# Kernel tuning notes

Hardware: AMD Instinct MI355X
Metric: run time of the kernel (lower is better)

## Reference

```python
import jax, jax.numpy as jnp
import numpy as np

D_IN = 2048
D_OUT = 2048
NUM_HEADS = 16
HEAD_DIM = D_OUT // NUM_HEADS  # 128
LATENT_DIM = 256
B, S = 2, 2048


def setup_inputs() -> dict:
    key = jax.random.key(0)
    ks = jax.random.split(key, 7)
    scale = 0.02
    return {
        "x": jax.random.normal(ks[0], (B, S, D_IN), dtype=jnp.float32),
        "W_query": jax.random.normal(ks[1], (D_IN, D_OUT), dtype=jnp.float32) * scale,
        "W_DKV": jax.random.normal(ks[2], (D_IN, LATENT_DIM), dtype=jnp.float32) * scale,
        "W_UKV": jax.random.normal(ks[3], (LATENT_DIM, 2 * D_OUT), dtype=jnp.float32) * scale,
        "W_out": jax.random.normal(ks[4], (D_OUT, D_IN), dtype=jnp.float32) * scale,
        "b_out": jax.random.normal(ks[5], (D_IN,), dtype=jnp.float32) * scale,
        "offset": 0,
    }


def reference(x, W_query, W_DKV, W_UKV, W_out, b_out, offset):
    Bq, Sq, _ = x.shape
    # projections
    q = x @ W_query                      # [B, S, d_out]
    latent = x @ W_DKV                   # [B, S, latent_dim]
    kv = latent @ W_UKV                  # [B, S, 2*d_out]
    k, v = jnp.split(kv, 2, axis=-1)     # each [B, S, d_out]

    def to_heads(t):
        return t.reshape(Bq, Sq, NUM_HEADS, HEAD_DIM).transpose(0, 2, 1, 3)  # [B, H, S, hd]

    qh, kh, vh = to_heads(q), to_heads(k), to_heads(v)

    scores = jnp.einsum("bhqd,bhkd->bhqk", qh, kh)  # [B, H, S, S]
    causal = jnp.tril(jnp.ones((Sq, Sq), dtype=bool))  # True = keep (kv_cache=None -> Sq==Skv)
    # faithful to original: masked_fill(-inf) BEFORE the rsqrt(head_dim) scaling
    scores = jnp.where(causal, scores, -jnp.inf)
    inv_sqrt_d = jax.lax.rsqrt(jnp.asarray(HEAD_DIM, dtype=scores.dtype))
    attn = jax.nn.softmax(scores * inv_sqrt_d, axis=-1)  # dropout p=0 -> identity

    ctx = jnp.einsum("bhqk,bhkd->bhqd", attn, vh)        # [B, H, S, hd]
    ctx = ctx.transpose(0, 2, 1, 3).reshape(Bq, Sq, D_OUT)
    return ctx @ W_out + b_out           # [B, S, d_in]
```

## Files before the change

### kernel.cpp

```cpp
#include <hip/hip_runtime.h>
#include <hip/hip_bf16.h>

typedef short bf16x8 __attribute__((ext_vector_type(8)));
typedef float f32x4 __attribute__((ext_vector_type(4)));
typedef float f32x16 __attribute__((ext_vector_type(16)));
typedef unsigned int u32x4 __attribute__((ext_vector_type(4)));
typedef unsigned short u16;
typedef unsigned short u16x4 __attribute__((ext_vector_type(4)));
typedef unsigned short u16x8 __attribute__((ext_vector_type(8)));

constexpr int D_IN = 2048, D_OUT = 2048, NH = 16, HD = 128, LAT = 256;
constexpr int Bb = 2, Ss = 2048, Mtot = Bb * Ss;

constexpr float QSCALE = 0.08838834764831845f * 1.4426950408889634f;
constexpr float NEG_BIG = -3.0e38f;

__device__ __forceinline__ u16 f2bf(float f) {
  unsigned u = __float_as_uint(f);
  unsigned r = ((u >> 16) & 1u) + 0x7fffu;
  return (u16)((u + r) >> 16);
}

__device__ __forceinline__ float bf2f(u16 v) {
  return __uint_as_float((unsigned)v << 16);
}

__device__ __forceinline__ float fexp2(float x) {
#if __has_builtin(__builtin_amdgcn_exp2f)
  return __builtin_amdgcn_exp2f(x);
#else
  return exp2f(x);
#endif
}

__device__ __forceinline__ unsigned cvtpk(float lo, float hi) {
  unsigned r;
  asm("v_cvt_pk_bf16_f32 %0, %1, %2" : "=v"(r) : "v"(lo), "v"(hi));
  return r;
}

__device__ __forceinline__ void swap32(unsigned& a, unsigned& b) {
  asm volatile("v_permlane32_swap_b32 %0, %1" : "+v"(a), "+v"(b));
}

__device__ __forceinline__ void gload_lds16(const u16* g, u16* l) {
  __builtin_amdgcn_global_load_lds((const __attribute__((address_space(1))) void*)g,
                                   (__attribute__((address_space(3))) void*)l, 16, 0, 0);
}

__global__ void k_cvt(const float* __restrict__ in, u16* __restrict__ out, int n) {
  int i = (blockIdx.x * blockDim.x + threadIdx.x) * 4;
  if (i >= n) return;
  float4 v = *reinterpret_cast<const float4*>(in + i);
  ushort4 o;
  o.x = f2bf(v.x); o.y = f2bf(v.y); o.z = f2bf(v.z); o.w = f2bf(v.w);
  *reinterpret_cast<ushort4*>(out + i) = o;
}

__global__ void k_tcvt_all(const float* __restrict__ w0, u16* __restrict__ o0,
                           const float* __restrict__ w1, u16* __restrict__ o1,
                           const float* __restrict__ w2, u16* __restrict__ o2,
                           const float* __restrict__ w3, u16* __restrict__ o3) {
  __shared__ float t[32][33];
  int id = blockIdx.x;
  const float* in;
  u16* out;
  int K, N, bx, by;
  if (id < 4096)      { in = w0; out = o0; K = 2048; N = 2048; bx = (id & 63) * 32; by = (id >> 6) * 32; }
  else if (id < 4608) { id -= 4096; in = w1; out = o1; K = 2048; N = 256;  bx = (id & 7) * 32;  by = (id >> 3) * 32; }
  else if (id < 5632) { id -= 4608; in = w2; out = o2; K = 256;  N = 4096; bx = (id & 127) * 32; by = (id >> 7) * 32; }
  else                { id -= 5632; in = w3; out = o3; K = 2048; N = 2048; bx = (id & 63) * 32; by = (id >> 6) * 32; }
  const int tx = threadIdx.x, ty = threadIdx.y;
#pragma unroll
  for (int j = 0; j < 32; j += 8)
    t[ty + j][tx] = in[(size_t)(by + ty + j) * N + bx + tx];
  __syncthreads();
#pragma unroll
  for (int j = 0; j < 32; j += 8)
    out[(size_t)(bx + ty + j) * K + by + tx] = f2bf(t[tx][ty + j]);
}

template <int OUT_MODE>
__global__ __launch_bounds__(256) void k_gemm(const u16* __restrict__ A,
                                              const u16* __restrict__ Bt,
                                              void* __restrict__ Cp,
                                              void* __restrict__ Cp2,
                                              const float* __restrict__ bias,
                                              float scale, int M, int N, int K) {
  constexpr int BK = 32;
  __shared__ u16 As[128 * BK];
  __shared__ u16 Bs[128 * BK];
  const int nwg = gridDim.x;
  int bid = blockIdx.x;
  bid = (bid & 7) * (nwg >> 3) + (bid >> 3);
  const int nbx = N >> 7;
  const int bx = bid % nbx, by = bid / nbx;
  const int row0 = by << 7, col0 = bx << 7;
  const int tid = threadIdx.x;
  const int wave = tid >> 6, lane = tid & 63;
  const int wr = (wave >> 1) * 64, wc = (wave & 1) * 64;
  const int lr = lane & 15, lg = lane >> 4;

  f32x4 acc[4][4];
#pragma unroll
  for (int m = 0; m < 4; ++m)
#pragma unroll
    for (int n = 0; n < 4; ++n) acc[m][n] = (f32x4)0.0f;

  const int crow = lane >> 2, ccol = (lane & 3) * 8;
  const u16* gA0 = A + (size_t)(row0 + wave * 32 + crow) * K + ccol;
  const u16* gA1 = gA0 + (size_t)16 * K;
  const u16* gB0 = Bt + (size_t)(col0 + wave * 32 + crow) * K + ccol;
  const u16* gB1 = gB0 + (size_t)16 * K;
  u16* lA0 = &As[(wave * 32) * BK];
  u16* lA1 = &As[(wave * 32 + 16) * BK];
  u16* lB0 = &Bs[(wave * 32) * BK];
  u16* lB1 = &Bs[(wave * 32 + 16) * BK];

  for (int k0 = 0; k0 < K; k0 += BK) {
    gload_lds16(gA0 + k0, lA0);
    gload_lds16(gA1 + k0, lA1);
    gload_lds16(gB0 + k0, lB0);
    gload_lds16(gB1 + k0, lB1);
    __syncthreads();
    bf16x8 af[4], bfr[4];
#pragma unroll
    for (int m = 0; m < 4; ++m)
      af[m] = *reinterpret_cast<const bf16x8*>(&As[(wr + m * 16 + lr) * BK + lg * 8]);
#pragma unroll
    for (int n = 0; n < 4; ++n)
      bfr[n] = *reinterpret_cast<const bf16x8*>(&Bs[(wc + n * 16 + lr) * BK + lg * 8]);
#pragma unroll
    for (int m = 0; m < 4; ++m)
#pragma unroll
      for (int n = 0; n < 4; ++n)
        acc[m][n] = __builtin_amdgcn_mfma_f32_16x16x32_bf16(af[m], bfr[n], acc[m][n], 0, 0, 0);
    __syncthreads();
  }

#pragma unroll
  for (int m = 0; m < 4; ++m) {
    const int r = row0 + wr + m * 16 + lg * 4;
#pragma unroll
    for (int n = 0; n < 4; ++n) {
      const int c = col0 + wc + n * 16 + lr;
#pragma unroll
      for (int i = 0; i < 4; ++i) {
        float v = acc[m][n][i];
        if (OUT_MODE == 0)
          ((u16*)Cp)[(size_t)(r + i) * N + c] = f2bf(v);
        else if (OUT_MODE == 1)
          ((float*)Cp)[(size_t)(r + i) * N + c] = v + bias[c];
        else {
          if (c < 2048)
            ((u16*)Cp)[(size_t)(r + i) * 2048 + c] = f2bf(v * scale);
          else
            ((u16*)Cp2)[(size_t)(r + i) * 256 + (c - 2048)] = f2bf(v);
        }
      }
    }
  }
}

__device__ __constant__ const signed char PT_qb[11] = {4,3,7,7,6,6,2,5,5,1,0};
__device__ __constant__ const signed char PT_k0[11] = {0,0,0,8,0,7,0,0,6,0,0};
__device__ __constant__ const signed char PT_k1[11] = {10,8,8,16,7,14,6,6,12,4,2};
__device__ __constant__ const signed char PT_md[11] = {0,0,1,2,1,2,0,1,2,0,0};

__global__ __launch_bounds__(512) void k_attn(const u16* __restrict__ Q,
                                              const u16* __restrict__ KV,
                                              u16* __restrict__ O,
                                              u16* __restrict__ o_part,
                                              float* __restrict__ lbuf) {
  __shared__ __align__(16) u16 Ks[128 * 128];
  __shared__ __align__(16) u16 Vt[128 * 128];
  const int p = blockIdx.x >> 5, bh = blockIdx.x & 31;
  const int qb = PT_qb[p], mode = PT_md[p];
  const int kt0 = PT_k0[p], kt1 = PT_k1[p];
  const int b = bh >> 4, h = bh & 15;
  const u16* Qb = Q + (size_t)b * Ss * D_OUT + h * HD;
  const u16* Kb = KV + (size_t)b * Ss * (2 * D_OUT) + h * HD;
  const u16* Vb = Kb + D_OUT;
  u16* Ob = O + (size_t)b * Ss * D_OUT + h * HD;

  const int tid = threadIdx.x, wave = tid >> 6, lane = tid & 63;
  const int lo = lane & 31, hi = lane >> 5;
  const int q0w = qb * 256 + wave * 32;

  bf16x8 qf[8];
  {
    const u16* qsrc = Qb + (size_t)(q0w + lo) * D_OUT + hi * 8;
#pragma unroll
    for (int ds = 0; ds < 8; ++ds)
      qf[ds] = *reinterpret_cast<const bf16x8*>(qsrc + ds * 16);
  }

  f32x16 ctx[4];
#pragma unroll
  for (int dt = 0; dt < 4; ++dt) ctx[dt] = (f32x16)0.0f;
  float lrow = 0.0f;

  const int sr = tid >> 2, sc = tid & 3;
  const int vk = (tid & 31) * 4, vd = (tid >> 5) * 8;
  const size_t kvstep = (size_t)128 * 2 * D_OUT;
  const u16* kg = Kb + (size_t)kt0 * kvstep + (size_t)sr * (2 * D_OUT) + sc * 8;
  const u16* vg = Vb + (size_t)kt0 * kvstep + (size_t)vk * (2 * D_OUT) + vd;

  const int ksw = (sr & 7) ^ (((sr >> 3) & 3) << 1);
  const int krd = ((lo & 7) * 8) ^ (((lo >> 3) & 3) << 4);

  int4 kreg[4];
  u16x8 vreg[4];
#pragma unroll
  for (int c = 0; c < 4; ++c) {
    kreg[c] = *reinterpret_cast<const int4*>(kg + c * 32);
    vreg[c] = *reinterpret_cast<const u16x8*>(vg + (size_t)c * (2 * D_OUT));
  }

  for (int kt = kt0; kt < kt1; ++kt) {
#pragma unroll
    for (int c = 0; c < 4; ++c)
      *reinterpret_cast<int4*>(&Ks[sr * 128 + (((sc + 4 * c) ^ ksw) * 8)]) = kreg[c];
#pragma unroll
    for (int jj = 0; jj < 8; ++jj) {
      u16x4 pk = {vreg[0][jj], vreg[1][jj], vreg[2][jj], vreg[3][jj]};
      *reinterpret_cast<u16x4*>(&Vt[(vd + jj) * 128 + (vk ^ (jj * 8))]) = pk;
    }
    if (kt + 1 < kt1) {
      const u16* kn = kg + (size_t)(kt + 1 - kt0) * kvstep;
      const u16* vn = vg + (size_t)(kt + 1 - kt0) * kvstep;
#pragma unroll
      for (int c = 0; c < 4; ++c) {
        kreg[c] = *reinterpret_cast<const int4*>(kn + c * 32);
        vreg[c] = *reinterpret_cast<const u16x8*>(vn + (size_t)c * (2 * D_OUT));
      }
    }
    __syncthreads();

#pragma unroll
    for (int sub = 0; sub < 2; ++sub) {
      const int kbs = kt * 128 + sub * 64;
      if (kbs <= q0w + 31) {
        f32x16 s0 = (f32x16)0.0f, s1 = (f32x16)0.0f;
        __builtin_amdgcn_s_setprio(1);
#pragma unroll
        for (int ds = 0; ds < 8; ++ds) {
          const int off = (16 * ds + 8 * hi) ^ krd;
          bf16x8 a0 = *reinterpret_cast<const bf16x8*>(&Ks[(sub * 64 + lo) * 128 + off]);
          bf16x8 a1 = *reinterpret_cast<const bf16x8*>(&Ks[(sub * 64 + 32 + lo) * 128 + off]);
          s0 = __builtin_amdgcn_mfma_f32_32x32x16_bf16(a0, qf[ds], s0, 0, 0, 0);
          s1 = __builtin_amdgcn_mfma_f32_32x32x16_bf16(a1, qf[ds], s1, 0, 0, 0);
        }
        __builtin_amdgcn_s_setprio(0);

        if (kbs + 63 > q0w) {
          const int qg = q0w + lo;
#pragma unroll
          for (int r = 0; r < 16; ++r) {
            const int koff = kbs + (r & 3) + 8 * (r >> 2) + 4 * hi;
            if (koff > qg) s0[r] = NEG_BIG;
            if (koff + 32 > qg) s1[r] = NEG_BIG;
          }
        }

#pragma unroll
        for (int r = 0; r < 16; ++r) s0[r] = fexp2(s0[r]);
#pragma unroll
        for (int r = 0; r < 16; ++r) s1[r] = fexp2(s1[r]);

        bf16x8 pa[4];
#pragma unroll
        for (int g = 0; g < 2; ++g) {
          const f32x16& sg = g ? s1 : s0;
#pragma unroll
          for (int half = 0; half < 2; ++half) {
            const int rb = half * 8;
            unsigned w0 = cvtpk(sg[rb + 0], sg[rb + 1]);
            unsigned w2 = cvtpk(sg[rb + 4], sg[rb + 5]);
            unsigned w1 = cvtpk(sg[rb + 2], sg[rb + 3]);
            unsigned w3 = cvtpk(sg[rb + 6], sg[rb + 7]);
            swap32(w0, w2);
            swap32(w1, w3);
            u32x4 fr = {w0, w1, w2, w3};
            pa[2 * g + half] = __builtin_bit_cast(bf16x8, fr);
          }
        }

        __builtin_amdgcn_s_setprio(1);
#pragma unroll
        for (int dt = 0; dt < 4; ++dt) {
          const int vrow = 32 * dt + lo;
#pragma unroll
          for (int ks = 0; ks < 4; ++ks) {
            const int off = sub * 64 + (((16 * ks + 8 * hi)) ^ ((lo & 7) * 8));
            bf16x8 bv = *reinterpret_cast<const bf16x8*>(&Vt[vrow * 128 + off]);
            ctx[dt] = __builtin_amdgcn_mfma_f32_32x32x16_bf16(pa[ks], bv, ctx[dt], 0, 0, 0);
          }
        }
        __builtin_amdgcn_s_setprio(0);

        float sm[16];
#pragma unroll
        for (int r = 0; r < 16; ++r) sm[r] = s0[r] + s1[r];
#pragma unroll
        for (int w = 8; w >= 1; w >>= 1)
#pragma unroll
          for (int r = 0; r < w; ++r) sm[r] += sm[r + w];
        lrow += sm[0] + __shfl_xor(sm[0], 32);
      }
    }
    __syncthreads();
  }

  if (mode == 0) {
    float linv = 1.0f / lrow;
#pragma unroll
    for (int r = 0; r < 16; ++r) {
      float lb = __shfl(linv, ((r & 3) + 8 * (r >> 2)) + 4 * hi);
      const int qr = q0w + (r & 3) + 8 * (r >> 2) + 4 * hi;
#pragma unroll
      for (int dt = 0; dt < 4; ++dt)
        Ob[(size_t)qr * D_OUT + dt * 32 + lo] = f2bf(ctx[dt][r] * lb);
    }
  } else {
    const int pi = bh * 6 + (qb - 5) * 2 + (mode - 1);
    u16* po = o_part + (size_t)pi * (256 * 128);
    float* pl = lbuf + (size_t)pi * 256;
#pragma unroll
    for (int r = 0; r < 16; ++r) {
      const int rl = wave * 32 + (r & 3) + 8 * (r >> 2) + 4 * hi;
#pragma unroll
      for (int dt = 0; dt < 4; ++dt)
        po[rl * 128 + dt * 32 + lo] = f2bf(ctx[dt][r]);
    }
    if (hi == 0) pl[wave * 32 + lo] = lrow;
  }
}

__global__ __launch_bounds__(256) void k_comb(const u16* __restrict__ o_part,
                                              const float* __restrict__ lbuf,
                                              u16* __restrict__ O) {
  const int sb = blockIdx.x >> 2;
  const int rg = blockIdx.x & 3;
  const int bh = sb / 3, js = sb % 3, qb = 5 + js;
  const int b = bh >> 4, h = bh & 15;
  u16* Ob = O + (size_t)b * Ss * D_OUT + h * HD;
  const int base = bh * 6 + js * 2;
  const u16* po0 = o_part + (size_t)base * (256 * 128);
  const u16* po1 = po0 + 256 * 128;
  const float* pl0 = lbuf + (size_t)base * 256;
  const float* pl1 = pl0 + 256;
  const int tid = threadIdx.x;
  const int r0 = tid >> 4, dg = (tid & 15) * 8;
#pragma unroll
  for (int rp = 0; rp < 4; ++rp) {
    const int row = rg * 64 + rp * 16 + r0;
    const float inv = 1.0f / (pl0[row] + pl1[row]);
    u16x8 o1 = *reinterpret_cast<const u16x8*>(po0 + row * 128 + dg);
    u16x8 o2 = *reinterpret_cast<const u16x8*>(po1 + row * 128 + dg);
    u16x8 o;
#pragma unroll
    for (int j = 0; j < 8; ++j)
      o[j] = f2bf((bf2f(o1[j]) + bf2f(o2[j])) * inv);
    *reinterpret_cast<u16x8*>(&Ob[(size_t)(qb * 256 + row) * D_OUT + dg]) = o;
  }
}

extern "C" void kernel_launch(void* const* d_in, const int* in_sizes, int n_in,
                              void* d_out, int out_size, void* d_ws, size_t ws_size,
                              hipStream_t stream) {
  const float* x    = (const float*)d_in[0];
  const float* Wq   = (const float*)d_in[1];
  const float* Wdkv = (const float*)d_in[2];
  const float* Wukv = (const float*)d_in[3];
  const float* Wout = (const float*)d_in[4];
  const float* bout = (const float*)d_in[5];
  float* out = (float*)d_out;

  char* ws = (char*)d_ws;
  size_t off = 0;
  auto alloc = [&](size_t bytes) -> void* {
    void* p = ws + off;
    off += (bytes + 255) & ~(size_t)255;
    return p;
  };
  u16* xb    = (u16*)alloc((size_t)Mtot * D_IN * 2);
  u16* wcat  = (u16*)alloc((size_t)(D_OUT + LAT) * D_IN * 2);
  u16* wukvT = (u16*)alloc((size_t)2 * D_OUT * LAT * 2);
  u16* woutT = (u16*)alloc((size_t)D_IN * D_OUT * 2);
  u16* q     = (u16*)alloc((size_t)Mtot * D_OUT * 2);
  u16* lat   = (u16*)alloc((size_t)Mtot * LAT * 2);
  u16* kv    = (u16*)alloc((size_t)Mtot * 2 * D_OUT * 2);
  u16* ctx   = (u16*)alloc((size_t)Mtot * D_OUT * 2);
  u16* opart = (u16*)alloc((size_t)192 * 256 * 128 * 2);
  float* lbp = (float*)alloc((size_t)192 * 256 * 4);

  {
    int n = Mtot * D_IN;
    k_cvt<<<n / 4 / 256, 256, 0, stream>>>(x, xb, n);
  }
  k_tcvt_all<<<dim3(9728), dim3(32, 8), 0, stream>>>(
      Wq, wcat, Wdkv, wcat + (size_t)D_OUT * D_IN, Wukv, wukvT, Wout, woutT);

  k_gemm<3><<<(Mtot / 128) * ((D_OUT + LAT) / 128), 256, 0, stream>>>(
      xb, wcat, q, lat, nullptr, QSCALE, Mtot, D_OUT + LAT, D_IN);
  k_gemm<0><<<(Mtot / 128) * (2 * D_OUT / 128), 256, 0, stream>>>(
      lat, wukvT, kv, nullptr, nullptr, 1.0f, Mtot, 2 * D_OUT, LAT);
  k_attn<<<dim3(11 * 32), 512, 0, stream>>>(q, kv, ctx, opart, lbp);
  k_comb<<<dim3(384), 256, 0, stream>>>(opart, lbp, ctx);
  k_gemm<1><<<(Mtot / 128) * (D_IN / 128), 256, 0, stream>>>(
      ctx, woutT, out, nullptr, bout, 1.0f, Mtot, D_IN, D_OUT);
}
```

Baseline: 235.8 us.

## Rewrite GEMM with 128x256 tiles, double-buffered LDS, XOR swizzle, interleaved prefetch

Replaces the 128x128 BK=32 GEMM with a 512-thread kernel that computes 128x256 tiles using BK=64 and double-buffered shared memory. Loads of the next K tile are interleaved with MFMA groups, and s_setprio raises priority around the MFMA groups. An XOR swizzle on LDS columns is meant to avoid bank conflicts. This aims to hide global load latency and cut the number of barriers, at the cost of more LDS per block (96KB), fewer workgroups, and more register pressure.

```diff
diff --git a/kernel.cpp b/kernel.cpp
--- a/kernel.cpp
+++ b/kernel.cpp
@@ -81,24 +81,23 @@
 }
 
 template <int OUT_MODE>
-__global__ __launch_bounds__(256) void k_gemm(const u16* __restrict__ A,
-                                              const u16* __restrict__ Bt,
-                                              void* __restrict__ Cp,
-                                              void* __restrict__ Cp2,
-                                              const float* __restrict__ bias,
-                                              float scale, int M, int N, int K) {
-  constexpr int BK = 32;
-  __shared__ u16 As[128 * BK];
-  __shared__ u16 Bs[128 * BK];
+__global__ __launch_bounds__(512) void k_gemm2(const u16* __restrict__ A,
+                                               const u16* __restrict__ Bt,
+                                               void* __restrict__ Cp,
+                                               void* __restrict__ Cp2,
+                                               const float* __restrict__ bias,
+                                               float scale, int M, int N, int K) {
+  __shared__ __align__(16) u16 As[2][128 * 64];
+  __shared__ __align__(16) u16 Bs[2][256 * 64];
   const int nwg = gridDim.x;
   int bid = blockIdx.x;
   bid = (bid & 7) * (nwg >> 3) + (bid >> 3);
-  const int nbx = N >> 7;
+  const int nbx = N >> 8;
   const int bx = bid % nbx, by = bid / nbx;
-  const int row0 = by << 7, col0 = bx << 7;
+  const int row0 = by << 7, col0 = bx << 8;
   const int tid = threadIdx.x;
   const int wave = tid >> 6, lane = tid & 63;
-  const int wr = (wave >> 1) * 64, wc = (wave & 1) * 64;
+  const int wm = wave >> 2, wn = wave & 3;
   const int lr = lane & 15, lg = lane >> 4;
 
   f32x4 acc[4][4];
@@ -107,43 +106,119 @@
 #pragma unroll
     for (int n = 0; n < 4; ++n) acc[m][n] = (f32x4)0.0f;
 
-  const int crow = lane >> 2, ccol = (lane & 3) * 8;
-  const u16* gA0 = A + (size_t)(row0 + wave * 32 + crow) * K + ccol;
-  const u16* gA1 = gA0 + (size_t)16 * K;
-  const u16* gB0 = Bt + (size_t)(col0 + wave * 32 + crow) * K + ccol;
-  const u16* gB1 = gB0 + (size_t)16 * K;
-  u16* lA0 = &As[(wave * 32) * BK];
-  u16* lA1 = &As[(wave * 32 + 16) * BK];
-  u16* lB0 = &Bs[(wave * 32) * BK];
-  u16* lB1 = &Bs[(wave * 32 + 16) * BK];
-
-  for (int k0 = 0; k0 < K; k0 += BK) {
-    gload_lds16(gA0 + k0, lA0);
-    gload_lds16(gA1 + k0, lA1);
-    gload_lds16(gB0 + k0, lB0);
-    gload_lds16(gB1 + k0, lB1);
+  const u16* asrc[2];
+  const u16* bsrc[4];
+#pragma unroll
+  for (int s = 0; s < 2; ++s) {
+    int p = s * 4096 + wave * 512 + lane * 8;
+    int row = p >> 6;
+    int col = (p & 63) ^ ((row & 7) << 3);
+    asrc[s] = A + (size_t)(row0 + row) * K + col;
+  }
+#pragma unroll
+  for (int s = 0; s < 4; ++s) {
+    int p = s * 4096 + wave * 512 + lane * 8;
+    int row = p >> 6;
+    int col = (p & 63) ^ ((row & 7) << 3);
+    bsrc[s] = Bt + (size_t)(col0 + row) * K + col;
+  }
+
+  const int NT = K >> 6;
+  const int rsw = (lr & 7) << 3;
+  const int arow = wm * 64;
+  const int brow = wn * 64;
+
+#pragma unroll
+  for (int s = 0; s < 2; ++s) gload_lds16(asrc[s], &As[0][s * 4096 + wave * 512]);
+#pragma unroll
+  for (int s = 0; s < 4; ++s) gload_lds16(bsrc[s], &Bs[0][s * 4096 + wave * 512]);
+  __syncthreads();
+
+  int b = 0;
+  for (int t = 0; t < NT; ++t) {
+    const bool pf = (t + 1 < NT);
+    const int ko = (t + 1) * 64;
+    const u16* ab = As[b];
+    const u16* bb = Bs[b];
+    u16* an = As[b ^ 1];
+    u16* bn = Bs[b ^ 1];
+
+    bf16x8 bfrag[4][2], afrag[2][2];
+    if (pf) {
+      gload_lds16(asrc[0] + ko, &an[0 * 4096 + wave * 512]);
+      gload_lds16(asrc[1] + ko, &an[1 * 4096 + wave * 512]);
+    }
+#pragma unroll
+    for (int n = 0; n < 4; ++n)
+#pragma unroll
+      for (int ks = 0; ks < 2; ++ks)
+        bfrag[n][ks] = *reinterpret_cast<const bf16x8*>(
+            &bb[(brow + n * 16 + lr) * 64 + ((ks * 32 + lg * 8) ^ rsw)]);
+#pragma unroll
+    for (int m = 0; m < 2; ++m)
+#pragma unroll
+      for (int ks = 0; ks < 2; ++ks)
+        afrag[m][ks] = *reinterpret_cast<const bf16x8*>(
+            &ab[(arow + m * 16 + lr) * 64 + ((ks * 32 + lg * 8) ^ rsw)]);
+    __builtin_amdgcn_s_setprio(1);
+#pragma unroll
+    for (int m = 0; m < 2; ++m)
+#pragma unroll
+      for (int n = 0; n < 2; ++n)
+#pragma unroll
+        for (int ks = 0; ks < 2; ++ks)
+          acc[m][n] = __builtin_amdgcn_mfma_f32_16x16x32_bf16(afrag[m][ks], bfrag[n][ks], acc[m][n], 0, 0, 0);
+    __builtin_amdgcn_s_setprio(0);
+    if (pf) {
+      gload_lds16(bsrc[0] + ko, &bn[0 * 4096 + wave * 512]);
+      gload_lds16(bsrc[1] + ko, &bn[1 * 4096 + wave * 512]);
+    }
+    __builtin_amdgcn_s_setprio(1);
+#pragma unroll
+    for (int m = 0; m < 2; ++m)
+#pragma unroll
+      for (int n = 2; n < 4; ++n)
+#pragma unroll
+        for (int ks = 0; ks < 2; ++ks)
+          acc[m][n] = __builtin_amdgcn_mfma_f32_16x16x32_bf16(afrag[m][ks], bfrag[n][ks], acc[m][n], 0, 0, 0);
+    __builtin_amdgcn_s_setprio(0);
+    if (pf) gload_lds16(bsrc[2] + ko, &bn[2 * 4096 + wave * 512]);
+#pragma unroll
+    for (int m = 0; m < 2; ++m)
+#pragma unroll
+      for (int ks = 0; ks < 2; ++ks)
+        afrag[m][ks] = *reinterpret_cast<const bf16x8*>(
+            &ab[(arow + (m + 2) * 16 + lr) * 64 + ((ks * 32 + lg * 8) ^ rsw)]);
+    __builtin_amdgcn_s_setprio(1);
+#pragma unroll
+    for (int m = 0; m < 2; ++m)
+#pragma unroll
+      for (int n = 0; n < 2; ++n)
+#pragma unroll
+        for (int ks = 0; ks < 2; ++ks)
+          acc[m + 2][n] = __builtin_amdgcn_mfma_f32_16x16x32_bf16(afrag[m][ks], bfrag[n][ks], acc[m + 2][n], 0, 0, 0);
+    __builtin_amdgcn_s_setprio(0);
+    if (pf) gload_lds16(bsrc[3] + ko, &bn[3 * 4096 + wave * 512]);
+    __builtin_amdgcn_s_setprio(1);
+#pragma unroll
+    for (int m = 0; m < 2; ++m)
+#pragma unroll
+      for (int n = 2; n < 4; ++n)
+#pragma unroll
+        for (int ks = 0; ks < 2; ++ks)
+          acc[m + 2][n] = __builtin_amdgcn_mfma_f32_16x16x32_bf16(afrag[m][ks], bfrag[n][ks], acc[m + 2][n], 0, 0, 0);
+    __builtin_amdgcn_s_setprio(0);
+
     __syncthreads();
-    bf16x8 af[4], bfr[4];
-#pragma unroll
-    for (int m = 0; m < 4; ++m)
-      af[m] = *reinterpret_cast<const bf16x8*>(&As[(wr + m * 16 + lr) * BK + lg * 8]);
-#pragma unroll
-    for (int n = 0; n < 4; ++n)
-      bfr[n] = *reinterpret_cast<const bf16x8*>(&Bs[(wc + n * 16 + lr) * BK + lg * 8]);
-#pragma unroll
-    for (int m = 0; m < 4; ++m)
-#pragma unroll
-      for (int n = 0; n < 4; ++n)
-        acc[m][n] = __builtin_amdgcn_mfma_f32_16x16x32_bf16(af[m], bfr[n], acc[m][n], 0, 0, 0);
-    __syncthreads();
+    b ^= 1;
   }
 
 #pragma unroll
   for (int m = 0; m < 4; ++m) {
-    const int r = row0 + wr + m * 16 + lg * 4;
+    const int r = row0 + wm * 64 + m * 16 + lg * 4;
 #pragma unroll
     for (int n = 0; n < 4; ++n) {
-      const int c = col0 + wc + n * 16 + lr;
+      const int c = col0 + wn * 64 + n * 16 + lr;
 #pragma unroll
       for (int i = 0; i < 4; ++i) {
         float v = acc[m][n][i];
@@ -402,12 +477,12 @@
   k_tcvt_all<<<dim3(9728), dim3(32, 8), 0, stream>>>(
       Wq, wcat, Wdkv, wcat + (size_t)D_OUT * D_IN, Wukv, wukvT, Wout, woutT);
 
-  k_gemm<3><<<(Mtot / 128) * ((D_OUT + LAT) / 128), 256, 0, stream>>>(
+  k_gemm2<3><<<(Mtot / 128) * ((D_OUT + LAT) / 256), 512, 0, stream>>>(
       xb, wcat, q, lat, nullptr, QSCALE, Mtot, D_OUT + LAT, D_IN);
-  k_gemm<0><<<(Mtot / 128) * (2 * D_OUT / 128), 256, 0, stream>>>(
+  k_gemm2<0><<<(Mtot / 128) * (2 * D_OUT / 256), 512, 0, stream>>>(
       lat, wukvT, kv, nullptr, nullptr, 1.0f, Mtot, 2 * D_OUT, LAT);
   k_attn<<<dim3(11 * 32), 512, 0, stream>>>(q, kv, ctx, opart, lbp);
   k_comb<<<dim3(384), 256, 0, stream>>>(opart, lbp, ctx);
-  k_gemm<1><<<(Mtot / 128) * (D_IN / 128), 256, 0, stream>>>(
+  k_gemm2<1><<<(Mtot / 128) * (D_IN / 256), 512, 0, stream>>>(
       ctx, woutT, out, nullptr, bout, 1.0f, Mtot, D_IN, D_OUT);
 }
```

Result: slower. 279.7 us (+18.6%).
